# Kernel tuning notes

Hardware: AMD Instinct MI355X
Metric: run time of the kernel (lower is better)

Reference implementation:

```python
import jax, jax.numpy as jnp
import numpy as np

M, NQ, NK, DZ, DX = 8, 1024, 1024, 256, 2
H, HD = 8, 32            # num_heads, head_dim
KH = 32                  # kernel MLP hidden width
INNER = H * HD           # 256


def setup_inputs() -> dict:
    key = jax.random.key(0)
    ks = jax.random.split(key, 12)
    f32 = jnp.float32
    return {
        "zq":  jax.random.normal(ks[0], (M, NQ, DZ), dtype=f32),
        "zk":  jax.random.normal(ks[1], (M, NK, DZ), dtype=f32),
        "zv":  jax.random.normal(ks[2], (M, NK, DZ), dtype=f32),
        "xq":  jax.random.normal(ks[3], (M, NQ, DX), dtype=f32),
        "xkv": jax.random.normal(ks[4], (M, NK, DX), dtype=f32),
        # projection weights (nn.Linear, bias=False); stored [in, out]
        "Wq":  jax.random.normal(ks[5], (DZ, INNER), dtype=f32) * 0.02,
        "Wk":  jax.random.normal(ks[6], (DZ, INNER), dtype=f32) * 0.02,
        "Wv":  jax.random.normal(ks[7], (DZ, INNER), dtype=f32) * 0.02,
        # output projection (Linear with bias; dropout p=0 -> identity)
        "Wout": jax.random.normal(ks[8], (INNER, DZ), dtype=f32) * 0.02,
        "bout": jnp.zeros((DZ,), dtype=f32),
        # kernel MLP: (dx + h) -> KH -> h
        "W1": jax.random.normal(ks[9], (DX + H, KH), dtype=f32) * 0.3,
        "b1": jnp.zeros((KH,), dtype=f32),
        "W2": jax.random.normal(ks[10], (KH, H), dtype=f32) * 0.3,
        "b2": jnp.zeros((H,), dtype=f32),
    }


def reference(zq, zk, zv, xq, xkv, Wq, Wk, Wv, Wout, bout, W1, b1, W2, b2):
    m, nq, _ = zq.shape
    nk = zk.shape[1]
    scale = HD ** -0.5

    # translation group action: pairwise position differences [m,nq,nk,dx]
    diff = xq[:, :, None, :] - xkv[:, None, :, :]

    q = (zq @ Wq).reshape(m, nq, H, HD)
    k = (zk @ Wk).reshape(m, nk, H, HD)
    v = (zv @ Wv).reshape(m, nk, H, HD)

    # token dots, already laid out as [m,nq,nk,h]
    token_dots = jnp.einsum("mqhd,mkhd->mqkh", q, k) * scale

    # kernel MLP over concatenated [diff, token_dots]: [m,nq,nk,dx+h] -> [m,nq,nk,h]
    kernel_input = jnp.concatenate([diff, token_dots], axis=-1)
    dots = jax.nn.relu(kernel_input @ W1 + b1) @ W2 + b2

    # softmax over keys (nk axis)
    attn = jax.nn.softmax(dots, axis=2)  # [m,nq,nk,h]

    out = jnp.einsum("mqkh,mkhd->mqhd", attn, v).reshape(m, nq, INNER)
    out = out @ Wout + bout

    # phi is None -> query locations pass through unchanged
    xq_new = xq
    return out, xq_new
```

## Files before the change

### kernel.cpp

```cpp
#include <hip/hip_runtime.h>

typedef float f32x4 __attribute__((ext_vector_type(4)));
typedef short s16x8 __attribute__((ext_vector_type(8)));
typedef unsigned short u16;
typedef unsigned int u32;

#define MFMA16 __builtin_amdgcn_mfma_f32_16x16x32_bf16
#define SCALE 0.17677669529663687f

__device__ __forceinline__ u16 f2b(float f) {
  union { float f; unsigned u; } x; x.f = f;
  unsigned r = x.u + 0x7fffu + ((x.u >> 16) & 1u);
  return (u16)(r >> 16);
}
__device__ __forceinline__ float b2f(u16 s) {
  union { unsigned u; float f; } x; x.u = ((unsigned)s) << 16;
  return x.f;
}
__device__ __forceinline__ u32 pkt(float a, float b) {
  return __builtin_amdgcn_perm(__builtin_bit_cast(u32, b),
                               __builtin_bit_cast(u32, a), 0x07060302u);
}
__device__ __forceinline__ u32 bperm(int idx, u32 src) {
  return (u32)__builtin_amdgcn_ds_bpermute(idx, (int)src);
}
__device__ __forceinline__ s16x8 mk8(u32 a, u32 b, u32 c, u32 d) {
  union { u32 w[4]; s16x8 v; } u;
  u.w[0] = a; u.w[1] = b; u.w[2] = c; u.w[3] = d;
  return u.v;
}

__global__ __launch_bounds__(256) void wtrans_kernel(
    const float* __restrict__ Wq, const float* __restrict__ Wk,
    const float* __restrict__ Wv, const float* __restrict__ Wo,
    u16* __restrict__ WqT, u16* __restrict__ WkT,
    u16* __restrict__ WvT, u16* __restrict__ WoT) {
  const float* src; u16* dst;
  switch (blockIdx.x) {
    case 0: src = Wq; dst = WqT; break;
    case 1: src = Wk; dst = WkT; break;
    case 2: src = Wv; dst = WvT; break;
    default: src = Wo; dst = WoT; break;
  }
  int j = blockIdx.y;
  int d = threadIdx.x;
  dst[j * 256 + d] = f2b(src[d * 256 + j]);
}

__global__ __launch_bounds__(256) void copyxq_kernel(const float* __restrict__ xq,
                                                     float* __restrict__ dst) {
  int i = blockIdx.x * 256 + threadIdx.x;
  dst[i] = xq[i];
}

__global__ __launch_bounds__(256) void proj_kernel(
    const float* __restrict__ zq, const float* __restrict__ zk,
    const float* __restrict__ zv,
    const u16* __restrict__ WqT, const u16* __restrict__ WkT,
    const u16* __restrict__ WvT,
    u16* __restrict__ qb, u16* __restrict__ kb, u16* __restrict__ vT) {
  const int mat = blockIdx.z;
  const float* Z = (mat == 0) ? zq : (mat == 1) ? zk : zv;
  const u16* WT = (mat == 0) ? WqT : (mat == 1) ? WkT : WvT;
  const int n0 = blockIdx.x * 64;
  const int j0 = blockIdx.y * 64;
  const int tid = threadIdx.x;
  const int lane = tid & 63, wid = tid >> 6;
  const int l15 = lane & 15, lg = lane >> 4;
  const int wn = wid & 1, wj = wid >> 1;

  __shared__ u16 As[64][40];
  __shared__ u16 Bs[64][40];

  f32x4 acc[2][2];
  #pragma unroll
  for (int a = 0; a < 2; ++a)
    #pragma unroll
    for (int b = 0; b < 2; ++b) acc[a][b] = (f32x4){0.f, 0.f, 0.f, 0.f};

  for (int ks = 0; ks < 8; ++ks) {
    const int d0 = ks * 32;
    const int r = tid >> 2, cb = (tid & 3) * 8;
    const float* zsrc = &Z[(size_t)(n0 + r) * 256 + d0 + cb];
    s16x8 t;
    #pragma unroll
    for (int j = 0; j < 8; ++j) t[j] = (short)f2b(zsrc[j]);
    *(s16x8*)&As[r][cb] = t;
    *(s16x8*)&Bs[r][cb] = *(const s16x8*)&WT[(size_t)(j0 + r) * 256 + d0 + cb];
    __syncthreads();
    s16x8 a0 = *(const s16x8*)&As[wn * 32 + l15][lg * 8];
    s16x8 a1 = *(const s16x8*)&As[wn * 32 + 16 + l15][lg * 8];
    s16x8 b0 = *(const s16x8*)&Bs[wj * 32 + l15][lg * 8];
    s16x8 b1 = *(const s16x8*)&Bs[wj * 32 + 16 + l15][lg * 8];
    acc[0][0] = MFMA16(a0, b0, acc[0][0], 0, 0, 0);
    acc[0][1] = MFMA16(a0, b1, acc[0][1], 0, 0, 0);
    acc[1][0] = MFMA16(a1, b0, acc[1][0], 0, 0, 0);
    acc[1][1] = MFMA16(a1, b1, acc[1][1], 0, 0, 0);
    __syncthreads();
  }
  #pragma unroll
  for (int sn = 0; sn < 2; ++sn)
    #pragma unroll
    for (int sj = 0; sj < 2; ++sj)
      #pragma unroll
      for (int i = 0; i < 4; ++i) {
        int n = n0 + wn * 32 + sn * 16 + lg * 4 + i;
        int j = j0 + wj * 32 + sj * 16 + l15;
        float av = acc[sn][sj][i];
        if (mat == 0) av *= SCALE;
        u16 val = f2b(av);
        if (mat == 0) {
          qb[(size_t)n * 256 + j] = val;
        } else if (mat == 1) {
          kb[(size_t)n * 256 + j] = val;
        } else {
          int mm = n >> 10, nn = n & 1023;
          vT[((size_t)(mm * 256 + j)) * 1024 + nn] = val;
        }
      }
}

__global__ __launch_bounds__(512, 4) void attn_kernel(
    const u16* __restrict__ qb, const u16* __restrict__ kb,
    const u16* __restrict__ vT,
    const float* __restrict__ xq, const float* __restrict__ xkv,
    const float* __restrict__ W1, const float* __restrict__ b1,
    const float* __restrict__ W2, const float* __restrict__ b2,
    u16* __restrict__ preP, float* __restrict__ Lb) {
  const int m = blockIdx.y;
  const int q0 = blockIdx.x * 16;
  const int kz = blockIdx.z;
  const int tid = threadIdx.x;
  const int lane = tid & 63;
  const int wid = tid >> 6;
  const int l15 = lane & 15;
  const int lg = lane >> 4;
  const int kk = wid * 16 + l15;

  u16* myPre = preP + (size_t)kz * (8192 * 256);
  float* myL = Lb + (size_t)kz * (8192 * 8);

  __shared__ u16 P_s[8][16][136];

  s16x8 w1a[2];
  #pragma unroll
  for (int cblk = 0; cblk < 2; ++cblk) {
    const int c = 8 * (l15 >> 2) + 4 * cblk + (l15 & 3);
    #pragma unroll
    for (int j = 0; j < 8; ++j) {
      const int dim = lg * 8 + j;
      u16 v = 0;
      if (dim < 10) v = f2b(W1[dim * 32 + c]);
      else if (dim == 10) v = f2b(b1[c]);
      w1a[cblk][j] = (short)v;
    }
  }
  s16x8 w2a;
  #pragma unroll
  for (int j = 0; j < 8; ++j) {
    const int c = lg * 8 + j;
    w2a[j] = (short)((l15 < 8) ? f2b(W2[c * 8 + l15]) : (u16)0);
  }
  float b2r[4];
  #pragma unroll
  for (int i = 0; i < 4; ++i) b2r[i] = b2[(lg & 1) * 4 + i];

  const int idx10 = (l15 + 0) * 4;
  const int idx11 = (l15 + 16) * 4;
  const int idx12 = (l15 + 32) * 4;
  const int idx13 = (l15 + 48) * 4;
  const u32 u1base = (lg == 1) ? 0x00003F80u : 0u;
  const bool lglo = (lg < 2);

  s16x8 ones;
  #pragma unroll
  for (int j = 0; j < 8; ++j) ones[j] = (l15 == 0) ? (short)0x3F80 : (short)0;

  s16x8 qfr[8];
  #pragma unroll
  for (int h = 0; h < 8; ++h)
    qfr[h] = *(const s16x8*)&qb[((size_t)(m * 1024 + q0 + l15)) * 256 + h * 32 + lg * 8];

  f32x4 acc_pv[2];
  acc_pv[0] = (f32x4){0.f, 0.f, 0.f, 0.f};
  acc_pv[1] = (f32x4){0.f, 0.f, 0.f, 0.f};
  f32x4 acc_sum = (f32x4){0.f, 0.f, 0.f, 0.f};
  const f32x4 Z4 = (f32x4){0.f, 0.f, 0.f, 0.f};

  for (int kt = 0; kt < 2; ++kt) {
    const int kg = kz * 256 + kt * 128;
    const float2 xk2 = *(const float2*)&xkv[((size_t)(m * 1024 + kg + kk)) * 2];

    u32 dpk[4][4];
    {
      f32x4 dacc[8];
      #pragma unroll
      for (int h = 0; h < 8; ++h) {
        const s16x8 b = *(const s16x8*)&kb[((size_t)(m * 1024 + kg + kk)) * 256 + h * 32 + lg * 8];
        dacc[h] = MFMA16(qfr[h], b, Z4, 0, 0, 0);
      }
      #pragma unroll
      for (int i = 0; i < 4; ++i)
        #pragma unroll
        for (int j = 0; j < 4; ++j)
          dpk[i][j] = pkt(dacc[2 * j][i], dacc[2 * j + 1][i]);
    }

    #pragma unroll 8
    for (int qg = 0; qg < 16; ++qg) {
      const int isrc = qg & 3;
      const int idxq = (qg >> 2) == 0 ? idx10 : (qg >> 2) == 1 ? idx11
                     : (qg >> 2) == 2 ? idx12 : idx13;
      const u32 p0 = bperm(idxq, dpk[isrc][0]);
      const u32 p1 = bperm(idxq, dpk[isrc][1]);
      const u32 p2 = bperm(idxq, dpk[isrc][2]);
      const u32 p3 = bperm(idxq, dpk[isrc][3]);
      const float2 xq2 = *(const float2*)&xq[((size_t)(m * 1024 + q0 + qg)) * 2];
      const u32 dqpair = pkt(xq2.x - xk2.x, xq2.y - xk2.y);
      const u32 u0 = (lg == 0) ? dqpair : ((lg == 1) ? p3 : 0u);
      const u32 u1 = (lg == 0) ? p0 : u1base;
      const u32 u2 = (lg == 0) ? p1 : 0u;
      const u32 u3 = (lg == 0) ? p2 : 0u;
      const s16x8 bf1 = mk8(u0, u1, u2, u3);
      const f32x4 h0 = MFMA16(w1a[0], bf1, Z4, 0, 0, 0);
      const f32x4 h1 = MFMA16(w1a[1], bf1, Z4, 0, 0, 0);
      const s16x8 bf2 = mk8(pkt(fmaxf(h0[0], 0.f), fmaxf(h0[1], 0.f)),
                            pkt(fmaxf(h0[2], 0.f), fmaxf(h0[3], 0.f)),
                            pkt(fmaxf(h1[0], 0.f), fmaxf(h1[1], 0.f)),
                            pkt(fmaxf(h1[2], 0.f), fmaxf(h1[3], 0.f)));
      const f32x4 Lg = MFMA16(w2a, bf2, Z4, 0, 0, 0);
      if (lglo) {
        #pragma unroll
        for (int i = 0; i < 4; ++i) {
          const float e = __expf(Lg[i] + b2r[i]);
          P_s[lg * 4 + i][qg][kk] = (u16)(__builtin_bit_cast(unsigned, e) >> 16);
        }
      }
    }
    __syncthreads();

    s16x8 pa[4];
    #pragma unroll
    for (int ks = 0; ks < 4; ++ks)
      pa[ks] = *(const s16x8*)&P_s[wid][l15][ks * 32 + lg * 8];
    #pragma unroll
    for (int dh = 0; dh < 2; ++dh) {
      const size_t vrow = ((size_t)(m * 256 + wid * 32 + dh * 16 + l15)) * 1024 + kg;
      #pragma unroll
      for (int ks = 0; ks < 4; ++ks) {
        const s16x8 b = *(const s16x8*)&vT[vrow + ks * 32 + lg * 8];
        acc_pv[dh] = MFMA16(pa[ks], b, acc_pv[dh], 0, 0, 0);
      }
    }
    #pragma unroll
    for (int ks = 0; ks < 4; ++ks)
      acc_sum = MFMA16(pa[ks], ones, acc_sum, 0, 0, 0);
    __syncthreads();
  }

  #pragma unroll
  for (int dh = 0; dh < 2; ++dh)
    #pragma unroll
    for (int i = 0; i < 4; ++i) {
      const int qr = lg * 4 + i;
      myPre[((size_t)(m * 1024 + q0 + qr)) * 256 + wid * 32 + dh * 16 + l15] = f2b(acc_pv[dh][i]);
    }
  if (l15 == 0) {
    #pragma unroll
    for (int i = 0; i < 4; ++i)
      myL[((size_t)(m * 1024 + q0 + lg * 4 + i)) * 8 + wid] = acc_sum[i];
  }
}

__global__ __launch_bounds__(256) void outp_kernel(
    const u16* __restrict__ preP, const float* __restrict__ Lb,
    const u16* __restrict__ WoT,
    const float* __restrict__ bout, float* __restrict__ out) {
  const int n0 = blockIdx.x * 64;
  const int j0 = blockIdx.y * 64;
  const int tid = threadIdx.x;
  const int lane = tid & 63, wid = tid >> 6;
  const int l15 = lane & 15, lg = lane >> 4;
  const int wn = wid & 1, wj = wid >> 1;
  __shared__ u16 As[64][40];
  __shared__ u16 Bs[64][40];
  f32x4 acc[2][2];
  #pragma unroll
  for (int a = 0; a < 2; ++a)
    #pragma unroll
    for (int b = 0; b < 2; ++b) acc[a][b] = (f32x4){0.f, 0.f, 0.f, 0.f};

  const size_t PSTRIDE = (size_t)8192 * 256;
  const size_t LSTRIDE = (size_t)8192 * 8;

  for (int ks = 0; ks < 8; ++ks) {
    const int d0 = ks * 32;
    const int r = tid >> 2, cb = (tid & 3) * 8;
    const size_t row = (size_t)(n0 + r);
    const float Ls = Lb[row * 8 + ks] + Lb[LSTRIDE + row * 8 + ks] +
                     Lb[2 * LSTRIDE + row * 8 + ks] + Lb[3 * LSTRIDE + row * 8 + ks];
    const float inv = 1.0f / Ls;
    const s16x8 p0 = *(const s16x8*)&preP[row * 256 + d0 + cb];
    const s16x8 p1 = *(const s16x8*)&preP[PSTRIDE + row * 256 + d0 + cb];
    const s16x8 p2 = *(const s16x8*)&preP[2 * PSTRIDE + row * 256 + d0 + cb];
    const s16x8 p3 = *(const s16x8*)&preP[3 * PSTRIDE + row * 256 + d0 + cb];
    s16x8 t;
    #pragma unroll
    for (int j = 0; j < 8; ++j) {
      const float v = (b2f((u16)p0[j]) + b2f((u16)p1[j]) + b2f((u16)p2[j]) + b2f((u16)p3[j])) * inv;
      t[j] = (short)f2b(v);
    }
    *(s16x8*)&As[r][cb] = t;
    *(s16x8*)&Bs[r][cb] = *(const s16x8*)&WoT[(size_t)(j0 + r) * 256 + d0 + cb];
    __syncthreads();
    s16x8 a0 = *(const s16x8*)&As[wn * 32 + l15][lg * 8];
    s16x8 a1 = *(const s16x8*)&As[wn * 32 + 16 + l15][lg * 8];
    s16x8 b0 = *(const s16x8*)&Bs[wj * 32 + l15][lg * 8];
    s16x8 b1 = *(const s16x8*)&Bs[wj * 32 + 16 + l15][lg * 8];
    acc[0][0] = MFMA16(a0, b0, acc[0][0], 0, 0, 0);
    acc[0][1] = MFMA16(a0, b1, acc[0][1], 0, 0, 0);
    acc[1][0] = MFMA16(a1, b0, acc[1][0], 0, 0, 0);
    acc[1][1] = MFMA16(a1, b1, acc[1][1], 0, 0, 0);
    __syncthreads();
  }
  #pragma unroll
  for (int sn = 0; sn < 2; ++sn)
    #pragma unroll
    for (int sj = 0; sj < 2; ++sj)
      #pragma unroll
      for (int i = 0; i < 4; ++i) {
        int n = n0 + wn * 32 + sn * 16 + lg * 4 + i;
        int j = j0 + wj * 32 + sj * 16 + l15;
        out[(size_t)n * 256 + j] = acc[sn][sj][i] + bout[j];
      }
}

extern "C" void kernel_launch(void* const* d_in, const int* in_sizes, int n_in,
                              void* d_out, int out_size, void* d_ws, size_t ws_size,
                              hipStream_t stream) {
  const float* zq = (const float*)d_in[0];
  const float* zk = (const float*)d_in[1];
  const float* zv = (const float*)d_in[2];
  const float* xq = (const float*)d_in[3];
  const float* xkv = (const float*)d_in[4];
  const float* Wq = (const float*)d_in[5];
  const float* Wk = (const float*)d_in[6];
  const float* Wv = (const float*)d_in[7];
  const float* Wo = (const float*)d_in[8];
  const float* bout = (const float*)d_in[9];
  const float* W1 = (const float*)d_in[10];
  const float* b1 = (const float*)d_in[11];
  const float* W2 = (const float*)d_in[12];
  const float* b2 = (const float*)d_in[13];
  float* out = (float*)d_out;

  const size_t MB = (size_t)1 << 20;
  char* ws = (char*)d_ws;
  u16* qb   = (u16*)(ws + 0 * MB);
  u16* kb   = (u16*)(ws + 4 * MB);
  u16* vT   = (u16*)(ws + 8 * MB);
  u16* preP = (u16*)(ws + 12 * MB);
  float* Lb = (float*)(ws + 28 * MB);
  u16* WqT  = (u16*)(ws + 29 * MB + 0 * (128 << 10));
  u16* WkT  = (u16*)(ws + 29 * MB + 1 * (128 << 10));
  u16* WvT  = (u16*)(ws + 29 * MB + 2 * (128 << 10));
  u16* WoT  = (u16*)(ws + 29 * MB + 3 * (128 << 10));

  wtrans_kernel<<<dim3(4, 256), dim3(256), 0, stream>>>(Wq, Wk, Wv, Wo, WqT, WkT, WvT, WoT);
  proj_kernel<<<dim3(128, 4, 3), dim3(256), 0, stream>>>(zq, zk, zv, WqT, WkT, WvT, qb, kb, vT);
  attn_kernel<<<dim3(64, 8, 4), dim3(512), 0, stream>>>(qb, kb, vT, xq, xkv, W1, b1, W2, b2, preP, Lb);
  outp_kernel<<<dim3(128, 4), dim3(256), 0, stream>>>(preP, Lb, WoT, bout, out);
  copyxq_kernel<<<dim3(64), dim3(256), 0, stream>>>(xq, out + (size_t)8 * 1024 * 256);
}
```

Baseline: 147.8 us.

## Restructure attention kernel to single-wave blocks with variable key split

Attention blocks shrink from 512 threads (8 waves sharing 128 keys) to a single 64-thread wave that walks its key range in 32-key superblocks and accumulates all 256 output dims in registers. The key split count becomes runtime-selected (8 when the workspace is large enough, otherwise 4), and the output kernel loops over that many partial results. The aim is more independent blocks, fewer large-block barriers and more parallelism across keys. In exchange Q fragments are reloaded from global for every 16 keys, each wave holds 16 accumulators, and with a split of 8 the partial buffers written and re-read double.

```diff
diff --git a/kernel.cpp b/kernel.cpp
--- a/kernel.cpp
+++ b/kernel.cpp
@@ -120,7 +120,7 @@
       }
 }
 
-__global__ __launch_bounds__(512, 4) void attn_kernel(
+__global__ __launch_bounds__(64, 3) void attn_kernel(
     const u16* __restrict__ qb, const u16* __restrict__ kb,
     const u16* __restrict__ vT,
     const float* __restrict__ xq, const float* __restrict__ xkv,
@@ -129,18 +129,17 @@
     u16* __restrict__ preP, float* __restrict__ Lb) {
   const int m = blockIdx.y;
   const int q0 = blockIdx.x * 16;
-  const int kz = blockIdx.z;
-  const int tid = threadIdx.x;
-  const int lane = tid & 63;
-  const int wid = tid >> 6;
+  const int kzi = blockIdx.z;
+  const int keys_per = 1024 / gridDim.z;
+  const int nsuper = keys_per >> 5;
+  const int lane = threadIdx.x & 63;
   const int l15 = lane & 15;
   const int lg = lane >> 4;
-  const int kk = wid * 16 + l15;
-
-  u16* myPre = preP + (size_t)kz * (8192 * 256);
-  float* myL = Lb + (size_t)kz * (8192 * 8);
-
-  __shared__ u16 P_s[8][16][136];
+
+  u16* myPre = preP + (size_t)kzi * (8192 * 256);
+  float* myL = Lb + (size_t)kzi * (8192 * 8);
+
+  __shared__ u16 P_s[8][16][40];
 
   s16x8 w1a[2];
   #pragma unroll
@@ -172,110 +171,109 @@
   const u32 u1base = (lg == 1) ? 0x00003F80u : 0u;
   const bool lglo = (lg < 2);
 
-  s16x8 ones;
-  #pragma unroll
-  for (int j = 0; j < 8; ++j) ones[j] = (l15 == 0) ? (short)0x3F80 : (short)0;
-
-  s16x8 qfr[8];
-  #pragma unroll
-  for (int h = 0; h < 8; ++h)
-    qfr[h] = *(const s16x8*)&qb[((size_t)(m * 1024 + q0 + l15)) * 256 + h * 32 + lg * 8];
-
-  f32x4 acc_pv[2];
-  acc_pv[0] = (f32x4){0.f, 0.f, 0.f, 0.f};
-  acc_pv[1] = (f32x4){0.f, 0.f, 0.f, 0.f};
-  f32x4 acc_sum = (f32x4){0.f, 0.f, 0.f, 0.f};
+  s16x8 onesA;
+  #pragma unroll
+  for (int j = 0; j < 8; ++j) onesA[j] = (short)0x3F80;
+
+  f32x4 acc2[16];
+  #pragma unroll
+  for (int dc = 0; dc < 16; ++dc) acc2[dc] = (f32x4){0.f, 0.f, 0.f, 0.f};
+  float Lacc[8];
+  #pragma unroll
+  for (int h = 0; h < 8; ++h) Lacc[h] = 0.0f;
   const f32x4 Z4 = (f32x4){0.f, 0.f, 0.f, 0.f};
 
-  for (int kt = 0; kt < 2; ++kt) {
-    const int kg = kz * 256 + kt * 128;
-    const float2 xk2 = *(const float2*)&xkv[((size_t)(m * 1024 + kg + kk)) * 2];
-
-    u32 dpk[4][4];
-    {
-      f32x4 dacc[8];
+  for (int sb = 0; sb < nsuper; ++sb) {
+    const int kgb = kzi * keys_per + sb * 32;
+    #pragma unroll
+    for (int half = 0; half < 2; ++half) {
+      const int kg = kgb + half * 16;
+      const float2 xk2 = *(const float2*)&xkv[((size_t)(m * 1024 + kg + l15)) * 2];
+
+      u32 dpk[4][4];
+      {
+        f32x4 dacc[8];
+        #pragma unroll
+        for (int h = 0; h < 8; ++h) {
+          const s16x8 a = *(const s16x8*)&qb[((size_t)(m * 1024 + q0 + l15)) * 256 + h * 32 + lg * 8];
+          const s16x8 b = *(const s16x8*)&kb[((size_t)(m * 1024 + kg + l15)) * 256 + h * 32 + lg * 8];
+          dacc[h] = MFMA16(a, b, Z4, 0, 0, 0);
+        }
+        #pragma unroll
+        for (int i = 0; i < 4; ++i)
+          #pragma unroll
+          for (int j = 0; j < 4; ++j)
+            dpk[i][j] = pkt(dacc[2 * j][i], dacc[2 * j + 1][i]);
+      }
+
       #pragma unroll
-      for (int h = 0; h < 8; ++h) {
-        const s16x8 b = *(const s16x8*)&kb[((size_t)(m * 1024 + kg + kk)) * 256 + h * 32 + lg * 8];
-        dacc[h] = MFMA16(qfr[h], b, Z4, 0, 0, 0);
-      }
-      #pragma unroll
-      for (int i = 0; i < 4; ++i)
-        #pragma unroll
-        for (int j = 0; j < 4; ++j)
-          dpk[i][j] = pkt(dacc[2 * j][i], dacc[2 * j + 1][i]);
-    }
-
-    #pragma unroll 8
-    for (int qg = 0; qg < 16; ++qg) {
-      const int isrc = qg & 3;
-      const int idxq = (qg >> 2) == 0 ? idx10 : (qg >> 2) == 1 ? idx11
-                     : (qg >> 2) == 2 ? idx12 : idx13;
-      const u32 p0 = bperm(idxq, dpk[isrc][0]);
-      const u32 p1 = bperm(idxq, dpk[isrc][1]);
-      const u32 p2 = bperm(idxq, dpk[isrc][2]);
-      const u32 p3 = bperm(idxq, dpk[isrc][3]);
-      const float2 xq2 = *(const float2*)&xq[((size_t)(m * 1024 + q0 + qg)) * 2];
-      const u32 dqpair = pkt(xq2.x - xk2.x, xq2.y - xk2.y);
-      const u32 u0 = (lg == 0) ? dqpair : ((lg == 1) ? p3 : 0u);
-      const u32 u1 = (lg == 0) ? p0 : u1base;
-      const u32 u2 = (lg == 0) ? p1 : 0u;
-      const u32 u3 = (lg == 0) ? p2 : 0u;
-      const s16x8 bf1 = mk8(u0, u1, u2, u3);
-      const f32x4 h0 = MFMA16(w1a[0], bf1, Z4, 0, 0, 0);
-      const f32x4 h1 = MFMA16(w1a[1], bf1, Z4, 0, 0, 0);
-      const s16x8 bf2 = mk8(pkt(fmaxf(h0[0], 0.f), fmaxf(h0[1], 0.f)),
-                            pkt(fmaxf(h0[2], 0.f), fmaxf(h0[3], 0.f)),
-                            pkt(fmaxf(h1[0], 0.f), fmaxf(h1[1], 0.f)),
-                            pkt(fmaxf(h1[2], 0.f), fmaxf(h1[3], 0.f)));
-      const f32x4 Lg = MFMA16(w2a, bf2, Z4, 0, 0, 0);
-      if (lglo) {
-        #pragma unroll
-        for (int i = 0; i < 4; ++i) {
-          const float e = __expf(Lg[i] + b2r[i]);
-          P_s[lg * 4 + i][qg][kk] = (u16)(__builtin_bit_cast(unsigned, e) >> 16);
+      for (int qg = 0; qg < 16; ++qg) {
+        const int isrc = qg & 3;
+        const int idxq = (qg >> 2) == 0 ? idx10 : (qg >> 2) == 1 ? idx11
+                       : (qg >> 2) == 2 ? idx12 : idx13;
+        const u32 p0 = bperm(idxq, dpk[isrc][0]);
+        const u32 p1 = bperm(idxq, dpk[isrc][1]);
+        const u32 p2 = bperm(idxq, dpk[isrc][2]);
+        const u32 p3 = bperm(idxq, dpk[isrc][3]);
+        const float2 xq2 = *(const float2*)&xq[((size_t)(m * 1024 + q0 + qg)) * 2];
+        const u32 dqpair = pkt(xq2.x - xk2.x, xq2.y - xk2.y);
+        const u32 u0 = (lg == 0) ? dqpair : ((lg == 1) ? p3 : 0u);
+        const u32 u1 = (lg == 0) ? p0 : u1base;
+        const u32 u2 = (lg == 0) ? p1 : 0u;
+        const u32 u3 = (lg == 0) ? p2 : 0u;
+        const s16x8 bf1 = mk8(u0, u1, u2, u3);
+        const f32x4 h0 = MFMA16(w1a[0], bf1, Z4, 0, 0, 0);
+        const f32x4 h1 = MFMA16(w1a[1], bf1, Z4, 0, 0, 0);
+        const s16x8 bf2 = mk8(pkt(fmaxf(h0[0], 0.f), fmaxf(h0[1], 0.f)),
+                              pkt(fmaxf(h0[2], 0.f), fmaxf(h0[3], 0.f)),
+                              pkt(fmaxf(h1[0], 0.f), fmaxf(h1[1], 0.f)),
+                              pkt(fmaxf(h1[2], 0.f), fmaxf(h1[3], 0.f)));
+        const f32x4 Lg = MFMA16(w2a, bf2, Z4, 0, 0, 0);
+        if (lglo) {
+          #pragma unroll
+          for (int i = 0; i < 4; ++i) {
+            const float e = __expf(Lg[i] + b2r[i]);
+            P_s[lg * 4 + i][qg][half * 16 + l15] =
+                (u16)(__builtin_bit_cast(unsigned, e) >> 16);
+          }
         }
       }
     }
     __syncthreads();
 
-    s16x8 pa[4];
-    #pragma unroll
-    for (int ks = 0; ks < 4; ++ks)
-      pa[ks] = *(const s16x8*)&P_s[wid][l15][ks * 32 + lg * 8];
-    #pragma unroll
-    for (int dh = 0; dh < 2; ++dh) {
-      const size_t vrow = ((size_t)(m * 256 + wid * 32 + dh * 16 + l15)) * 1024 + kg;
-      #pragma unroll
-      for (int ks = 0; ks < 4; ++ks) {
-        const s16x8 b = *(const s16x8*)&vT[vrow + ks * 32 + lg * 8];
-        acc_pv[dh] = MFMA16(pa[ks], b, acc_pv[dh], 0, 0, 0);
-      }
-    }
-    #pragma unroll
-    for (int ks = 0; ks < 4; ++ks)
-      acc_sum = MFMA16(pa[ks], ones, acc_sum, 0, 0, 0);
-    __syncthreads();
-  }
-
-  #pragma unroll
-  for (int dh = 0; dh < 2; ++dh)
-    #pragma unroll
-    for (int i = 0; i < 4; ++i) {
-      const int qr = lg * 4 + i;
-      myPre[((size_t)(m * 1024 + q0 + qr)) * 256 + wid * 32 + dh * 16 + l15] = f2b(acc_pv[dh][i]);
-    }
-  if (l15 == 0) {
+    s16x8 paf[8];
+    #pragma unroll
+    for (int h = 0; h < 8; ++h)
+      paf[h] = *(const s16x8*)&P_s[h][l15][lg * 8];
+    #pragma unroll
+    for (int dc = 0; dc < 16; ++dc) {
+      const s16x8 bv = *(const s16x8*)&vT[((size_t)(m * 256 + dc * 16 + l15)) * 1024 + kgb + lg * 8];
+      acc2[dc] = MFMA16(paf[dc >> 1], bv, acc2[dc], 0, 0, 0);
+    }
+    #pragma unroll
+    for (int h = 0; h < 8; ++h) {
+      const f32x4 lc = MFMA16(onesA, paf[h], Z4, 0, 0, 0);
+      Lacc[h] += lc[0];
+    }
+    __syncthreads();
+  }
+
+  #pragma unroll
+  for (int dc = 0; dc < 16; ++dc)
     #pragma unroll
     for (int i = 0; i < 4; ++i)
-      myL[((size_t)(m * 1024 + q0 + lg * 4 + i)) * 8 + wid] = acc_sum[i];
+      myPre[((size_t)(m * 1024 + q0 + lg * 4 + i)) * 256 + dc * 16 + l15] = f2b(acc2[dc][i]);
+  if (lg == 0) {
+    #pragma unroll
+    for (int h = 0; h < 8; ++h)
+      myL[((size_t)(m * 1024 + q0 + l15)) * 8 + h] = Lacc[h];
   }
 }
 
 __global__ __launch_bounds__(256) void outp_kernel(
     const u16* __restrict__ preP, const float* __restrict__ Lb,
     const u16* __restrict__ WoT,
-    const float* __restrict__ bout, float* __restrict__ out) {
+    const float* __restrict__ bout, float* __restrict__ out, int kz) {
   const int n0 = blockIdx.x * 64;
   const int j0 = blockIdx.y * 64;
   const int tid = threadIdx.x;
@@ -297,19 +295,18 @@
     const int d0 = ks * 32;
     const int r = tid >> 2, cb = (tid & 3) * 8;
     const size_t row = (size_t)(n0 + r);
-    const float Ls = Lb[row * 8 + ks] + Lb[LSTRIDE + row * 8 + ks] +
-                     Lb[2 * LSTRIDE + row * 8 + ks] + Lb[3 * LSTRIDE + row * 8 + ks];
+    float Ls = 0.0f;
+    for (int s = 0; s < kz; ++s) Ls += Lb[s * LSTRIDE + row * 8 + ks];
     const float inv = 1.0f / Ls;
-    const s16x8 p0 = *(const s16x8*)&preP[row * 256 + d0 + cb];
-    const s16x8 p1 = *(const s16x8*)&preP[PSTRIDE + row * 256 + d0 + cb];
-    const s16x8 p2 = *(const s16x8*)&preP[2 * PSTRIDE + row * 256 + d0 + cb];
-    const s16x8 p3 = *(const s16x8*)&preP[3 * PSTRIDE + row * 256 + d0 + cb];
+    float a8[8] = {0.f, 0.f, 0.f, 0.f, 0.f, 0.f, 0.f, 0.f};
+    for (int s = 0; s < kz; ++s) {
+      const s16x8 p = *(const s16x8*)&preP[s * PSTRIDE + row * 256 + d0 + cb];
+      #pragma unroll
+      for (int j = 0; j < 8; ++j) a8[j] += b2f((u16)p[j]);
+    }
     s16x8 t;
     #pragma unroll
-    for (int j = 0; j < 8; ++j) {
-      const float v = (b2f((u16)p0[j]) + b2f((u16)p1[j]) + b2f((u16)p2[j]) + b2f((u16)p3[j])) * inv;
-      t[j] = (short)f2b(v);
-    }
+    for (int j = 0; j < 8; ++j) t[j] = (short)f2b(a8[j] * inv);
     *(s16x8*)&As[r][cb] = t;
     *(s16x8*)&Bs[r][cb] = *(const s16x8*)&WoT[(size_t)(j0 + r) * 256 + d0 + cb];
     __syncthreads();
@@ -355,20 +352,22 @@
   float* out = (float*)d_out;
 
   const size_t MB = (size_t)1 << 20;
+  const int KZ = (ws_size >= 48 * MB) ? 8 : 4;
   char* ws = (char*)d_ws;
   u16* qb   = (u16*)(ws + 0 * MB);
   u16* kb   = (u16*)(ws + 4 * MB);
   u16* vT   = (u16*)(ws + 8 * MB);
   u16* preP = (u16*)(ws + 12 * MB);
-  float* Lb = (float*)(ws + 28 * MB);
-  u16* WqT  = (u16*)(ws + 29 * MB + 0 * (128 << 10));
-  u16* WkT  = (u16*)(ws + 29 * MB + 1 * (128 << 10));
-  u16* WvT  = (u16*)(ws + 29 * MB + 2 * (128 << 10));
-  u16* WoT  = (u16*)(ws + 29 * MB + 3 * (128 << 10));
+  float* Lb = (float*)(ws + (12 + (size_t)KZ * 4) * MB);
+  char* wbase = ws + (12 + (size_t)KZ * 4) * MB + (size_t)KZ * (256 << 10);
+  u16* WqT  = (u16*)(wbase + 0 * (128 << 10));
+  u16* WkT  = (u16*)(wbase + 1 * (128 << 10));
+  u16* WvT  = (u16*)(wbase + 2 * (128 << 10));
+  u16* WoT  = (u16*)(wbase + 3 * (128 << 10));
 
   wtrans_kernel<<<dim3(4, 256), dim3(256), 0, stream>>>(Wq, Wk, Wv, Wo, WqT, WkT, WvT, WoT);
   proj_kernel<<<dim3(128, 4, 3), dim3(256), 0, stream>>>(zq, zk, zv, WqT, WkT, WvT, qb, kb, vT);
-  attn_kernel<<<dim3(64, 8, 4), dim3(512), 0, stream>>>(qb, kb, vT, xq, xkv, W1, b1, W2, b2, preP, Lb);
-  outp_kernel<<<dim3(128, 4), dim3(256), 0, stream>>>(preP, Lb, WoT, bout, out);
+  attn_kernel<<<dim3(64, 8, KZ), dim3(64), 0, stream>>>(qb, kb, vT, xq, xkv, W1, b1, W2, b2, preP, Lb);
+  outp_kernel<<<dim3(128, 4), dim3(256), 0, stream>>>(preP, Lb, WoT, bout, out, KZ);
   copyxq_kernel<<<dim3(64), dim3(256), 0, stream>>>(xq, out + (size_t)8 * 1024 * 256);
 }
```

New measurement: 193.2 us. 1.31x slower.
